# Performance work log

Hardware: AMD Instinct MI355X
Metric: run time of the kernel (lower is better)

## Reference

```python
import jax, jax.numpy as jnp
import numpy as np

IN_C, OUT_C, EDGE_C = 128, 64, 1
N_NODES, N_EDGES = 50000, 800000


def setup_inputs() -> dict:
    key = jax.random.key(0)
    ks = jax.random.split(key, 12)
    d = OUT_C
    # xavier-uniform-ish scales
    def xav(k, shape):
        lim = float(np.sqrt(6.0 / (shape[0] + shape[1])))
        return jax.random.uniform(k, shape, jnp.float32, -lim, lim)
    return {
        "feat_src": jax.random.normal(ks[0], (N_NODES, IN_C), jnp.float32),
        "feat_dst": jax.random.normal(ks[1], (N_NODES, IN_C), jnp.float32),
        "edge_weight": jax.random.uniform(ks[2], (N_EDGES, EDGE_C), jnp.float32),
        "src_idx": jax.random.randint(ks[3], (N_EDGES,), 0, N_NODES),
        "dst_idx": jnp.sort(jax.random.randint(ks[4], (N_EDGES,), 0, N_NODES)),
        "weight_n": xav(ks[5], (IN_C, d)),
        "weight_e": xav(ks[6], (EDGE_C, d)),
        "query": xav(ks[7], (d, d)),
        "key_w": xav(ks[8], (d, d)),
        "att_w": xav(ks[9], (3 * d, 1)),
        "att_b": jnp.zeros((1,), jnp.float32),
        "out_w": xav(ks[10], (2 * d, d)),
        "out_b": jnp.zeros((d,), jnp.float32),
    }


def reference(feat_src, feat_dst, edge_weight, src_idx, dst_idx,
              weight_n, weight_e, query, key_w, att_w, att_b, out_w, out_b):
    d = query.shape[0]
    n_dst = feat_dst.shape[0]
    h_src = feat_src @ weight_n                      # [N_src, d]
    h_dst = feat_dst @ weight_n                      # [N_dst, d]
    edge_emb = edge_weight @ weight_e                # [E, d]
    q_e = (h_dst @ query)[dst_idx]                   # [E, d] gather
    k_e = (h_src @ key_w)[src_idx]                   # [E, d] gather
    # linear_att(concat([q, k, e])) without materializing the concat
    logits = (q_e @ att_w[:d] + k_e @ att_w[d:2 * d]
              + edge_emb @ att_w[2 * d:] + att_b)    # [E, 1]
    logits = jax.nn.leaky_relu(logits, 0.2)
    # segment softmax over destination nodes
    m = jax.ops.segment_max(logits, dst_idx, num_segments=n_dst)   # [N_dst, 1]
    ex = jnp.exp(logits - m[dst_idx])
    s = jax.ops.segment_sum(ex, dst_idx, num_segments=n_dst)       # [N_dst, 1]
    alpha = ex / (s[dst_idx] + 1e-16)                # [E, 1]
    msg = alpha * h_src[src_idx]                     # [E, d]
    agg = jax.ops.segment_sum(msg, dst_idx, num_segments=n_dst)    # [N_dst, d]
    # linear_out(concat([h_dst, agg]))
    out = h_dst @ out_w[:d] + agg @ out_w[d:] + out_b
    return out
```

## Files before the change

### kernel.cpp

```cpp
#include <hip/hip_runtime.h>
#include <hip/hip_bf16.h>

typedef short short8 __attribute__((ext_vector_type(8)));
typedef float float4v __attribute__((ext_vector_type(4)));
typedef unsigned short ushort4v __attribute__((ext_vector_type(4)));

static __device__ __forceinline__ short f2b(float f) {
    union { __hip_bfloat16 b; short s; } v;
    v.b = __float2bfloat16(f);
    return v.s;
}
static __device__ __forceinline__ float b2f(unsigned short u) {
    union { float f; unsigned v; } x;
    x.v = ((unsigned)u) << 16;
    return x.f;
}

__global__ void __launch_bounds__(256) setup_kernel(
    const float* __restrict__ query, const float* __restrict__ key_w,
    const float* __restrict__ weight_e, const float* __restrict__ att_w,
    const float* __restrict__ Wn, const float* __restrict__ out_w,
    const int* __restrict__ dst_idx,
    unsigned short* __restrict__ BTs, unsigned short* __restrict__ BTd,
    float* __restrict__ Wk, float* __restrict__ Wq, float* __restrict__ escale,
    int* __restrict__ row_ptr, int n_nodes, int n_edges) {
    int b = blockIdx.x, t = threadIdx.x;
    if (b < 64) {
        int idx = b * 256 + t;
        int mat = idx >> 13;
        int rem = idx & 8191;
        int n = rem >> 7, k = rem & 127;
        float s = 0.f;
        for (int m = 0; m < 64; ++m)
            s += Wn[k * 64 + m] * out_w[(mat ? m : 64 + m) * 64 + n];
        (mat ? BTd : BTs)[n * 128 + k] = (unsigned short)f2b(s);
    } else if (b == 64) {
        __shared__ float kq[128];
        __shared__ float ep[64];
        if (t < 64) {
            float s = 0.f;
            for (int j = 0; j < 64; ++j) s += key_w[t * 64 + j] * att_w[64 + j];
            kq[t] = s;
        } else if (t < 128) {
            int i = t - 64;
            float s = 0.f;
            for (int j = 0; j < 64; ++j) s += query[i * 64 + j] * att_w[j];
            kq[64 + i] = s;
        } else if (t < 192) {
            int j = t - 128;
            ep[j] = weight_e[j] * att_w[128 + j];
        }
        __syncthreads();
        if (t < 128) {
            float s = 0.f;
            for (int k = 0; k < 64; ++k) s += Wn[t * 64 + k] * kq[k];
            Wk[t] = s;
        } else {
            int i = t - 128;
            float s = 0.f;
            for (int k = 0; k < 64; ++k) s += Wn[i * 64 + k] * kq[64 + k];
            Wq[i] = s;
        }
        if (t == 0) {
            float s = 0.f;
            for (int j = 0; j < 64; ++j) s += ep[j];
            escale[0] = s;
        }
    } else {
        int idx = (b - 65) * 256 + t;
        if (idx > n_nodes) return;
        int lo = 0, hi = n_edges;
        while (lo < hi) {
            int mid = (lo + hi) >> 1;
            if (dst_idx[mid] < idx) lo = mid + 1; else hi = mid;
        }
        row_ptr[idx] = lo;
    }
}

__global__ void __launch_bounds__(256) gemm_kernel(
    const float* __restrict__ feat_src, const float* __restrict__ feat_dst,
    const unsigned short* __restrict__ BTs, const unsigned short* __restrict__ BTd,
    const float* __restrict__ Wk, const float* __restrict__ Wq,
    unsigned short* __restrict__ hw2, float* __restrict__ out,
    const float* __restrict__ out_b, float* __restrict__ kscore,
    float* __restrict__ qscore, int n_nodes, int nb) {
    __shared__ __align__(16) unsigned short BT[64 * 136];
    int t = threadIdx.x;
    bool isSrc = (int)blockIdx.x < nb;
    int bs = isSrc ? blockIdx.x : blockIdx.x - nb;
    int wave = t >> 6, lane = t & 63;
    int m15 = lane & 15, quad = lane >> 4;

    int rb = bs * 64 + wave * 16;
    bool valid = rb < n_nodes;

    const float* A = isSrc ? feat_src : feat_dst;
    float4v a0[4], a1[4];
    if (valid) {
        const float* Arow = A + (size_t)(rb + m15) * 128 + quad * 8;
#pragma unroll
        for (int kk = 0; kk < 4; ++kk) {
            a0[kk] = *(const float4v*)(Arow + kk * 32);
            a1[kk] = *(const float4v*)(Arow + kk * 32 + 4);
        }
    }

    const unsigned short* BTg = isSrc ? BTs : BTd;
#pragma unroll
    for (int i = 0; i < 4; ++i) {
        int j = i * 256 + t;
        int n = j >> 4, k8 = (j & 15) * 8;
        *(short8*)(&BT[n * 136 + k8]) = *(const short8*)(BTg + n * 128 + k8);
    }
    __syncthreads();
    if (!valid) return;

    const float* w = isSrc ? Wk : Wq;
    float4v acc[4] = {};
    float sk = 0.f;
#pragma unroll
    for (int kk = 0; kk < 4; ++kk) {
        float4v w0 = *(const float4v*)(w + kk * 32 + quad * 8);
        float4v w1 = *(const float4v*)(w + kk * 32 + quad * 8 + 4);
#pragma unroll
        for (int j = 0; j < 4; ++j) sk += a0[kk][j] * w0[j] + a1[kk][j] * w1[j];
        short8 a;
#pragma unroll
        for (int j = 0; j < 4; ++j) { a[j] = f2b(a0[kk][j]); a[4 + j] = f2b(a1[kk][j]); }
#pragma unroll
        for (int nt = 0; nt < 4; ++nt) {
            short8 bb = *(const short8*)(&BT[(nt * 16 + m15) * 136 + kk * 32 + quad * 8]);
            acc[nt] = __builtin_amdgcn_mfma_f32_16x16x32_bf16(a, bb, acc[nt], 0, 0, 0);
        }
    }
#pragma unroll
    for (int nt = 0; nt < 4; ++nt) {
        int col = nt * 16 + m15;
        float bv = isSrc ? 0.f : out_b[col];
#pragma unroll
        for (int r = 0; r < 4; ++r) {
            int row = rb + quad * 4 + r;
            if (isSrc) hw2[(size_t)row * 64 + col] = (unsigned short)f2b(acc[nt][r]);
            else       out[(size_t)row * 64 + col] = acc[nt][r] + bv;
        }
    }
    sk += __shfl_xor(sk, 16);
    sk += __shfl_xor(sk, 32);
    if (quad == 0) {
        if (isSrc) kscore[rb + m15] = sk;
        else       qscore[rb + m15] = sk;
    }
}

__global__ void __launch_bounds__(256) agg_kernel(
    const int* __restrict__ src_idx, const float* __restrict__ edge_w,
    const unsigned short* __restrict__ hw2, const float* __restrict__ kscore,
    const float* __restrict__ qscore, const float* __restrict__ escale_p,
    const float* __restrict__ att_b, const int* __restrict__ row_ptr,
    float* __restrict__ out, int n_nodes) {
    int wid = (int)((blockIdx.x * blockDim.x + threadIdx.x) >> 6);
    int lane = threadIdx.x & 63;
    int n0 = wid * 2;
    if (n0 >= n_nodes) return;
    int nCnt = (n0 + 1 < n_nodes) ? 2 : 1;
    int rp0 = row_ptr[n0];
    int rp1 = row_ptr[n0 + 1];
    int rp2 = (nCnt == 2) ? row_ptr[n0 + 2] : rp1;
    int total = rp2 - rp0;
    if (total == 0) return;
    float escale = escale_p[0];
    float bias = att_b[0];
    int eslot = lane >> 4, cg = lane & 15;

    if (total <= 64) {
        int m = rp1 - rp0;
        int s0 = 0; float w = 0.f;
        if (lane < total) {
            s0 = src_idx[rp0 + lane];
            float lg = qscore[n0 + (lane >= m ? 1 : 0)] + kscore[s0]
                     + edge_w[rp0 + lane] * escale + bias;
            lg = (lg > 0.f) ? lg : 0.2f * lg;
            w = __expf(fminf(lg, 80.f));
        }
        float pre = w;
#pragma unroll
        for (int off = 1; off < 64; off <<= 1) {
            float tv = __shfl_up(pre, off);
            if (lane >= off) pre += tv;
        }
        float sumAll = __shfl(pre, 63);
        float sum0 = (m > 0) ? __shfl(pre, m - 1) : 0.f;
        float sum1 = sumAll - sum0;
        float mySum = (lane >= m) ? sum1 : sum0;
        float alpha0 = w * (1.f / (mySum + 1e-16f));

        for (int j = 0; j < nCnt; ++j) {
            int sl = j ? m : 0;
            int deg = j ? (total - m) : m;
            if (deg == 0) continue;
            float ac0 = 0.f, ac1 = 0.f, ac2 = 0.f, ac3 = 0.f;
            for (int b = 0; b < deg; b += 4) {
                int eo = b + eslot;
                int idx = (eo < deg) ? (sl + eo) : sl;
                float alpha = __shfl(alpha0, idx);
                int s = __shfl(s0, idx);
                if (eo >= deg) alpha = 0.f;
                ushort4v h = *(const ushort4v*)(hw2 + (size_t)s * 64 + cg * 4);
                ac0 += alpha * b2f(h[0]);
                ac1 += alpha * b2f(h[1]);
                ac2 += alpha * b2f(h[2]);
                ac3 += alpha * b2f(h[3]);
            }
            ac0 += __shfl_xor(ac0, 16); ac0 += __shfl_xor(ac0, 32);
            ac1 += __shfl_xor(ac1, 16); ac1 += __shfl_xor(ac1, 32);
            ac2 += __shfl_xor(ac2, 16); ac2 += __shfl_xor(ac2, 32);
            ac3 += __shfl_xor(ac3, 16); ac3 += __shfl_xor(ac3, 32);
            if (lane < 16) {
                float* op = out + (size_t)(n0 + j) * 64 + lane * 4;
                float4v bb = *(const float4v*)op;
                bb[0] += ac0; bb[1] += ac1; bb[2] += ac2; bb[3] += ac3;
                *(float4v*)op = bb;
            }
        }
    } else {
        for (int j = 0; j < nCnt; ++j) {
            int start = (j == 0) ? rp0 : rp1;
            int deg = ((j == 0) ? rp1 : rp2) - start;
            if (deg == 0) continue;
            float qs = qscore[n0 + j];
            float ac0 = 0.f, ac1 = 0.f, ac2 = 0.f, ac3 = 0.f;
            if (deg <= 64) {
                int s0 = 0; float lg0 = -1e30f;
                if (lane < deg) {
                    s0 = src_idx[start + lane];
                    float lg = qs + kscore[s0] + edge_w[start + lane] * escale + bias;
                    lg0 = (lg > 0.f) ? lg : 0.2f * lg;
                }
                float mx = lg0;
#pragma unroll
                for (int off = 32; off; off >>= 1) mx = fmaxf(mx, __shfl_xor(mx, off));
                float a0 = __expf(lg0 - mx);
                float sm = a0;
#pragma unroll
                for (int off = 32; off; off >>= 1) sm += __shfl_xor(sm, off);
                float alpha0 = a0 * (1.f / (sm + 1e-16f));
                for (int b = 0; b < deg; b += 4) {
                    int eo = b + eslot;
                    int idx = (eo < deg) ? eo : 0;
                    float alpha = __shfl(alpha0, idx);
                    int s = __shfl(s0, idx);
                    if (eo >= deg) alpha = 0.f;
                    ushort4v h = *(const ushort4v*)(hw2 + (size_t)s * 64 + cg * 4);
                    ac0 += alpha * b2f(h[0]);
                    ac1 += alpha * b2f(h[1]);
                    ac2 += alpha * b2f(h[2]);
                    ac3 += alpha * b2f(h[3]);
                }
            } else {
                float mx = -1e30f, sm = 0.f;
                for (int eo = lane; eo < deg; eo += 64) {
                    int s = src_idx[start + eo];
                    float lg = qs + kscore[s] + edge_w[start + eo] * escale + bias;
                    lg = (lg > 0.f) ? lg : 0.2f * lg;
                    float nm = fmaxf(mx, lg);
                    sm = sm * __expf(mx - nm) + __expf(lg - nm);
                    mx = nm;
                }
                for (int off = 32; off; off >>= 1) {
                    float m2 = __shfl_xor(mx, off);
                    float s2 = __shfl_xor(sm, off);
                    float nm = fmaxf(mx, m2);
                    sm = sm * __expf(mx - nm) + s2 * __expf(m2 - nm);
                    mx = nm;
                }
                float inv = 1.f / (sm + 1e-16f);
                for (int b = 0; b < deg; b += 4) {
                    int eo = b + eslot;
                    bool valid = eo < deg;
                    int e = start + (valid ? eo : 0);
                    int s = src_idx[e];
                    float lg = qs + kscore[s] + edge_w[e] * escale + bias;
                    lg = (lg > 0.f) ? lg : 0.2f * lg;
                    float alpha = valid ? __expf(lg - mx) * inv : 0.f;
                    ushort4v h = *(const ushort4v*)(hw2 + (size_t)s * 64 + cg * 4);
                    ac0 += alpha * b2f(h[0]);
                    ac1 += alpha * b2f(h[1]);
                    ac2 += alpha * b2f(h[2]);
                    ac3 += alpha * b2f(h[3]);
                }
            }
            ac0 += __shfl_xor(ac0, 16); ac0 += __shfl_xor(ac0, 32);
            ac1 += __shfl_xor(ac1, 16); ac1 += __shfl_xor(ac1, 32);
            ac2 += __shfl_xor(ac2, 16); ac2 += __shfl_xor(ac2, 32);
            ac3 += __shfl_xor(ac3, 16); ac3 += __shfl_xor(ac3, 32);
            if (lane < 16) {
                float* op = out + (size_t)(n0 + j) * 64 + lane * 4;
                float4v bb = *(const float4v*)op;
                bb[0] += ac0; bb[1] += ac1; bb[2] += ac2; bb[3] += ac3;
                *(float4v*)op = bb;
            }
        }
    }
}

extern "C" void kernel_launch(void* const* d_in, const int* in_sizes, int n_in,
                              void* d_out, int out_size, void* d_ws, size_t ws_size,
                              hipStream_t stream) {
    const float* feat_src = (const float*)d_in[0];
    const float* feat_dst = (const float*)d_in[1];
    const float* edge_w   = (const float*)d_in[2];
    const int*   src_idx  = (const int*)d_in[3];
    const int*   dst_idx  = (const int*)d_in[4];
    const float* weight_n = (const float*)d_in[5];
    const float* weight_e = (const float*)d_in[6];
    const float* query    = (const float*)d_in[7];
    const float* key_w    = (const float*)d_in[8];
    const float* att_w    = (const float*)d_in[9];
    const float* att_b    = (const float*)d_in[10];
    const float* out_w    = (const float*)d_in[11];
    const float* out_b    = (const float*)d_in[12];
    float* out = (float*)d_out;

    int n_nodes = in_sizes[0] / 128;
    int n_edges = in_sizes[3];

    char* p = (char*)d_ws;
    unsigned short* hw2 = (unsigned short*)p;  p += (size_t)n_nodes * 64 * 2;
    float* kscore = (float*)p;  p += (size_t)n_nodes * 4;
    float* qscore = (float*)p;  p += (size_t)n_nodes * 4;
    unsigned short* BTs = (unsigned short*)p;  p += 64 * 128 * 2;
    unsigned short* BTd = (unsigned short*)p;  p += 64 * 128 * 2;
    float* Wk     = (float*)p;  p += 128 * 4;
    float* Wq     = (float*)p;  p += 128 * 4;
    float* escale = (float*)p;  p += 64;
    int*  row_ptr = (int*)p;

    int rp_blocks = (n_nodes + 1 + 255) / 256;
    hipLaunchKernelGGL(setup_kernel, dim3(65 + rp_blocks), dim3(256), 0, stream,
                       query, key_w, weight_e, att_w, weight_n, out_w, dst_idx,
                       BTs, BTd, Wk, Wq, escale, row_ptr, n_nodes, n_edges);

    int nb = (n_nodes + 63) / 64;
    hipLaunchKernelGGL(gemm_kernel, dim3(2 * nb), dim3(256), 0, stream,
                       feat_src, feat_dst, BTs, BTd, Wk, Wq,
                       hw2, out, out_b, kscore, qscore, n_nodes, nb);

    int n_waves = (n_nodes + 1) / 2;
    hipLaunchKernelGGL(agg_kernel, dim3((n_waves + 3) / 4), dim3(256), 0, stream,
                       src_idx, edge_w, hw2, kscore, qscore,
                       escale, att_b, row_ptr, out, n_nodes);
}
```

Measured before the change: 154.3 us.

## Process three destination nodes per wavefront and unroll gather loop by two

The aggregation kernel now packs three destination nodes per 64-lane wavefront instead of two, so one segmented prefix scan covers up to three segments when their combined degree fits in 64 lanes. The inner gather loop handles two edge groups per iteration, which puts two independent row loads in flight. This aims to make better use of the lanes, since the average degree is about 16 and two nodes use only about half the wave, and to expose more memory-level parallelism. In exchange there are fewer waves in total, which may lower occupancy and latency hiding, and more edges fall into the slower path when the combined degree exceeds 64.

```diff
diff --git a/kernel.cpp b/kernel.cpp
--- a/kernel.cpp
+++ b/kernel.cpp
@@ -161,25 +161,28 @@
     float* __restrict__ out, int n_nodes) {
     int wid = (int)((blockIdx.x * blockDim.x + threadIdx.x) >> 6);
     int lane = threadIdx.x & 63;
-    int n0 = wid * 2;
+    int n0 = wid * 3;
     if (n0 >= n_nodes) return;
-    int nCnt = (n0 + 1 < n_nodes) ? 2 : 1;
-    int rp0 = row_ptr[n0];
-    int rp1 = row_ptr[n0 + 1];
-    int rp2 = (nCnt == 2) ? row_ptr[n0 + 2] : rp1;
-    int total = rp2 - rp0;
+    int nCnt = n_nodes - n0; if (nCnt > 3) nCnt = 3;
+    int rp[4];
+    rp[0] = row_ptr[n0];
+#pragma unroll
+    for (int j = 1; j <= 3; ++j) rp[j] = (j <= nCnt) ? row_ptr[n0 + j] : 0;
+    int total = rp[nCnt] - rp[0];
     if (total == 0) return;
     float escale = escale_p[0];
     float bias = att_b[0];
     int eslot = lane >> 4, cg = lane & 15;
 
     if (total <= 64) {
-        int m = rp1 - rp0;
-        int s0 = 0; float w = 0.f;
+        int m1 = rp[1] - rp[0];
+        int m2 = (nCnt >= 2) ? rp[2] - rp[0] : m1;
+        int sv = 0; float w = 0.f;
         if (lane < total) {
-            s0 = src_idx[rp0 + lane];
-            float lg = qscore[n0 + (lane >= m ? 1 : 0)] + kscore[s0]
-                     + edge_w[rp0 + lane] * escale + bias;
+            int nid = (lane >= m2) ? 2 : (lane >= m1 ? 1 : 0);
+            sv = src_idx[rp[0] + lane];
+            float lg = qscore[n0 + nid] + kscore[sv]
+                     + edge_w[rp[0] + lane] * escale + bias;
             lg = (lg > 0.f) ? lg : 0.2f * lg;
             w = __expf(fminf(lg, 80.f));
         }
@@ -189,28 +192,34 @@
             float tv = __shfl_up(pre, off);
             if (lane >= off) pre += tv;
         }
-        float sumAll = __shfl(pre, 63);
-        float sum0 = (m > 0) ? __shfl(pre, m - 1) : 0.f;
-        float sum1 = sumAll - sum0;
-        float mySum = (lane >= m) ? sum1 : sum0;
+        float preA = (m1 > 0) ? __shfl(pre, m1 - 1) : 0.f;
+        float preB = (m2 > 0) ? __shfl(pre, m2 - 1) : 0.f;
+        float preC = __shfl(pre, total - 1);
+        float sumA = preA, sumB = preB - preA, sumC = preC - preB;
+        float mySum = (lane >= m2) ? sumC : ((lane >= m1) ? sumB : sumA);
         float alpha0 = w * (1.f / (mySum + 1e-16f));
 
+        int sl[3] = {0, m1, m2};
+        int dg[3] = {m1, m2 - m1, total - m2};
         for (int j = 0; j < nCnt; ++j) {
-            int sl = j ? m : 0;
-            int deg = j ? (total - m) : m;
+            int deg = dg[j];
             if (deg == 0) continue;
+            int base0 = sl[j];
             float ac0 = 0.f, ac1 = 0.f, ac2 = 0.f, ac3 = 0.f;
-            for (int b = 0; b < deg; b += 4) {
-                int eo = b + eslot;
-                int idx = (eo < deg) ? (sl + eo) : sl;
-                float alpha = __shfl(alpha0, idx);
-                int s = __shfl(s0, idx);
-                if (eo >= deg) alpha = 0.f;
-                ushort4v h = *(const ushort4v*)(hw2 + (size_t)s * 64 + cg * 4);
-                ac0 += alpha * b2f(h[0]);
-                ac1 += alpha * b2f(h[1]);
-                ac2 += alpha * b2f(h[2]);
-                ac3 += alpha * b2f(h[3]);
+            for (int b = 0; b < deg; b += 8) {
+                int eo0 = b + eslot, eo1 = b + 4 + eslot;
+                int i0 = (eo0 < deg) ? (base0 + eo0) : base0;
+                int i1 = (eo1 < deg) ? (base0 + eo1) : base0;
+                float al0 = __shfl(alpha0, i0); if (eo0 >= deg) al0 = 0.f;
+                float al1 = __shfl(alpha0, i1); if (eo1 >= deg) al1 = 0.f;
+                int sg0 = __shfl(sv, i0);
+                int sg1 = __shfl(sv, i1);
+                ushort4v h0 = *(const ushort4v*)(hw2 + (size_t)sg0 * 64 + cg * 4);
+                ushort4v h1 = *(const ushort4v*)(hw2 + (size_t)sg1 * 64 + cg * 4);
+                ac0 += al0 * b2f(h0[0]) + al1 * b2f(h1[0]);
+                ac1 += al0 * b2f(h0[1]) + al1 * b2f(h1[1]);
+                ac2 += al0 * b2f(h0[2]) + al1 * b2f(h1[2]);
+                ac3 += al0 * b2f(h0[3]) + al1 * b2f(h1[3]);
             }
             ac0 += __shfl_xor(ac0, 16); ac0 += __shfl_xor(ac0, 32);
             ac1 += __shfl_xor(ac1, 16); ac1 += __shfl_xor(ac1, 32);
@@ -225,8 +234,8 @@
         }
     } else {
         for (int j = 0; j < nCnt; ++j) {
-            int start = (j == 0) ? rp0 : rp1;
-            int deg = ((j == 0) ? rp1 : rp2) - start;
+            int start = rp[j];
+            int deg = rp[j + 1] - start;
             if (deg == 0) continue;
             float qs = qscore[n0 + j];
             float ac0 = 0.f, ac1 = 0.f, ac2 = 0.f, ac3 = 0.f;
@@ -346,7 +355,7 @@
                        feat_src, feat_dst, BTs, BTd, Wk, Wq,
                        hw2, out, out_b, kscore, qscore, n_nodes, nb);
 
-    int n_waves = (n_nodes + 1) / 2;
+    int n_waves = (n_nodes + 2) / 3;
     hipLaunchKernelGGL(agg_kernel, dim3((n_waves + 3) / 4), dim3(256), 0, stream,
                        src_idx, edge_w, hw2, kscore, qscore,
                        escale, att_b, row_ptr, out, n_nodes);
```

Result: no change. 156.0 us (+1.1%).
